# Kernel optimization log

Measured on AMD Instinct MI355X. Metric: run time of the kernel, lower is better.

The kernel has to match this reference:

```python
import jax, jax.numpy as jnp
import numpy as np

P = 8.0  # Lp exponent of the distance neuron (finite-p stage of l_inf-dist training)


def _patches(t, k, stride, pad):
    # [B, Cin, H, W] -> [B, Cin*k*k, H', W'], feature dim ordered channel-major
    return jax.lax.conv_general_dilated_patches(
        t, (k, k), (stride, stride), [(pad, pad), (pad, pad)])


def _lp(d):
    # d: [B, Cout, Cin*k*k, H', W'] nonnegative -> Lp norm over patch dim
    return jnp.power(jnp.sum(jnp.power(d, P), axis=2), 1.0 / P)


def norm_dist_conv(x, l, u, w, stride, pad):
    # Lp-distance "convolution": y[b,o,i,j] = || patch(x)[b,:,i,j] - w[o,:] ||_p
    # mean_normalize=True: zero-center each output unit's weight vector
    Cout, Cin, k, _ = w.shape
    wf = w.reshape(Cout, -1)
    wf = wf - jnp.mean(wf, axis=1, keepdims=True)
    wb = wf[None, :, :, None, None]                      # [1, Cout, Ckk, 1, 1]
    px = _patches(x, k, stride, pad)[:, None]            # [B, 1, Ckk, H', W']
    pl = _patches(l, k, stride, pad)[:, None]
    pu = _patches(u, k, stride, pad)[:, None]
    y = _lp(jnp.abs(px - wb))
    # interval bounds of |x_j - w_j| given x_j in [l_j, u_j], then monotone Lp
    dl = jnp.maximum(jnp.maximum(pl - wb, wb - pu), 0.0)
    du = jnp.maximum(jnp.abs(pl - wb), jnp.abs(pu - wb))
    return y, _lp(dl), _lp(du)


def bound_relu(x, l, u):
    # ReLU is monotone: apply elementwise to value and both bounds
    return jax.nn.relu(x), jax.nn.relu(l), jax.nn.relu(u)


def setup_inputs() -> dict:
    key = jax.random.key(0)
    k1, k2, k3 = jax.random.split(key, 3)
    B, C, H, W = 4, 32, 32, 32
    eps = 0.1  # l_inf perturbation radius
    x = jax.random.normal(k1, (B, C, H, W), dtype=jnp.float32)
    lower = x - eps
    upper = x + eps
    scale = 1.0 / np.sqrt(C * 9)
    weight1 = jax.random.normal(k2, (C, C, 3, 3), dtype=jnp.float32) * scale
    weight2 = jax.random.normal(k3, (C, C, 3, 3), dtype=jnp.float32) * scale
    return {"x": x, "lower": lower, "upper": upper,
            "weight1": weight1, "weight2": weight2}


def reference(x, lower, upper, weight1, weight2):
    # conv1 (stride=1, pad=1) -> BoundReLU -> conv2 -> residual add -> BoundReLU
    o = norm_dist_conv(x, lower, upper, weight1, 1, 1)
    o = bound_relu(*o)
    o = norm_dist_conv(*o, weight2, 1, 1)
    out = (o[0] + x, o[1] + lower, o[2] + upper)  # identity shortcut (stride=1, in==out)
    out = bound_relu(*out)
    return jnp.stack(out)  # [3, B, C, H, W]: (value, lower, upper)
```

## Files before the change

### kernel.cpp

```cpp
#include <hip/hip_runtime.h>

#define NB 4
#define NC 32
#define NH 32
#define NW 32
#define KK 288
#define PLANE (NB*NC*NH*NW)
#define CQ 8

typedef float v2f __attribute__((ext_vector_type(2)));

__device__ __forceinline__ float s3(float v) { return sqrtf(sqrtf(sqrtf(v))); }
__device__ __forceinline__ v2f pkfma(v2f a, v2f b, v2f c) { return __builtin_elementwise_fma(a, b, c); }
__device__ __forceinline__ v2f pkmax(v2f a, v2f b) { return __builtin_elementwise_max(a, b); }

__global__ __launch_bounds__(256) void prep_weights_k(
        const float* __restrict__ w1, const float* __restrict__ w2,
        float* __restrict__ wf1, float* __restrict__ wf2)
{
    const int row = blockIdx.x;
    const float* src = (row < NC) ? w1 : w2;
    float* dst = (row < NC) ? wf1 : wf2;
    const int co = row & (NC - 1);
    const int tid = threadIdx.x;
    __shared__ float red[256];
    const float a = src[co*KK + tid];
    const float b = (tid + 256 < KK) ? src[co*KK + tid + 256] : 0.0f;
    red[tid] = a + b;
    __syncthreads();
    for (int s = 128; s > 0; s >>= 1) {
        if (tid < s) red[tid] += red[tid + s];
        __syncthreads();
    }
    const float mean = red[0] * (1.0f / (float)KK);
    const int q    = ((co >> 4) << 3) | (co & 7);
    const int slot = (co >> 3) & 1;
    {
        const int e = tid, c = e / 9, r9 = e - c*9, r = r9 / 3, kw = r9 - r*3;
        dst[((q*NC + c)*3 + r)*8 + kw*2 + slot] = a - mean;
    }
    if (tid + 256 < KK) {
        const int e = tid + 256, c = e / 9, r9 = e - c*9, r = r9 / 3, kw = r9 - r*3;
        dst[((q*NC + c)*3 + r)*8 + kw*2 + slot] = b - mean;
    }
}

template<bool STAGE2>
__global__ __launch_bounds__(256, 2) void normdist_conv_k(
    const float* __restrict__ sy,
    const float* __restrict__ sl,
    const float* __restrict__ su,
    const float* __restrict__ wf,
    float* __restrict__ pY, float* __restrict__ pL, float* __restrict__ pU)
{
    const int h    = blockIdx.x;
    const int cq   = blockIdx.y;
    const int cq0  = cq * CQ;
    const int b    = blockIdx.z;
    const int tid  = threadIdx.x;
    const int wv   = tid >> 6;
    const int lane = tid & 63;
    const int ps   = lane >> 4;
    const int pp   = lane & 15;
    const int p0   = pp * 2;

    __shared__ float4 sP[CQ*3*34];

    for (int i = tid; i < CQ*3*34; i += 256) {
        const int c   = i / 102;
        const int rem = i - c*102;
        const int r   = rem / 34;
        const int col = rem - r*34;
        const int gh  = h + r - 1;
        const int gw  = col - 1;
        float vx = 0.0f, vl = 0.0f, vu = 0.0f;
        if ((unsigned)gh < NH && (unsigned)gw < NW) {
            const int g = ((b*NC + cq0 + c)*NH + gh)*NW + gw;
            if (STAGE2) {
                vx = s3(sy[g] + sy[PLANE + g] + sy[2*PLANE + g] + sy[3*PLANE + g]);
                vl = s3(sl[g] + sl[PLANE + g] + sl[2*PLANE + g] + sl[3*PLANE + g]);
                vu = s3(su[g] + su[PLANE + g] + su[2*PLANE + g] + su[3*PLANE + g]);
            } else {
                vx = sy[g]; vl = sl[g]; vu = su[g];
            }
        }
        sP[i] = make_float4(vx, vl, vu, 0.0f);
    }
    __syncthreads();

    const int q = wv*4 + ps;
    const float4* wq = (const float4*)wf + (q*NC + cq0)*6;

    v2f aY0 = {0,0}, aL0 = {0,0}, aU0 = {0,0};
    v2f aY1 = {0,0}, aL1 = {0,0}, aU1 = {0,0};

    auto tap2 = [&](v2f w, const float4& p, v2f& aY, v2f& aL, v2f& aU) {
        const v2f P  = {p.x, p.x};
        const v2f Lo = {p.y, p.y};
        const v2f Up = {p.z, p.z};
        const v2f d  = P - w;
        const v2f d2 = d*d, d4 = d2*d2;
        aY = pkfma(d4, d4, aY);
        const v2f a  = Lo - w;
        const v2f nb = w - Up;
        const v2f z  = {0.0f, 0.0f};
        const v2f m  = pkmax(pkmax(a, nb), z);
        const v2f m2 = m*m, m4 = m2*m2;
        aL = pkfma(m4, m4, aL);
        const v2f a2 = a*a, q2 = nb*nb;
        const v2f mm2 = pkmax(a2, q2);
        const v2f mm4 = mm2*mm2;
        aU = pkfma(mm4, mm4, aU);
    };

    for (int c = 0; c < CQ; ++c) {
        const int pb = c*102 + p0;
        const float4 p00 = sP[pb +  0], p01 = sP[pb +  1], p02 = sP[pb +  2], p03 = sP[pb +  3];
        const float4 p10 = sP[pb + 34], p11 = sP[pb + 35], p12 = sP[pb + 36], p13 = sP[pb + 37];
        const float4 p20 = sP[pb + 68], p21 = sP[pb + 69], p22 = sP[pb + 70], p23 = sP[pb + 71];

        const float4 w0lo = wq[c*6+0], w0hi = wq[c*6+1];
        const float4 w1lo = wq[c*6+2], w1hi = wq[c*6+3];
        const float4 w2lo = wq[c*6+4], w2hi = wq[c*6+5];

        const v2f w00 = {w0lo.x, w0lo.y}, w01 = {w0lo.z, w0lo.w}, w02 = {w0hi.x, w0hi.y};
        const v2f w10 = {w1lo.x, w1lo.y}, w11 = {w1lo.z, w1lo.w}, w12 = {w1hi.x, w1hi.y};
        const v2f w20 = {w2lo.x, w2lo.y}, w21 = {w2lo.z, w2lo.w}, w22 = {w2hi.x, w2hi.y};

        tap2(w00, p00, aY0, aL0, aU0); tap2(w01, p01, aY0, aL0, aU0); tap2(w02, p02, aY0, aL0, aU0);
        tap2(w10, p10, aY0, aL0, aU0); tap2(w11, p11, aY0, aL0, aU0); tap2(w12, p12, aY0, aL0, aU0);
        tap2(w20, p20, aY0, aL0, aU0); tap2(w21, p21, aY0, aL0, aU0); tap2(w22, p22, aY0, aL0, aU0);
        tap2(w00, p01, aY1, aL1, aU1); tap2(w01, p02, aY1, aL1, aU1); tap2(w02, p03, aY1, aL1, aU1);
        tap2(w10, p11, aY1, aL1, aU1); tap2(w11, p12, aY1, aL1, aU1); tap2(w12, p13, aY1, aL1, aU1);
        tap2(w20, p21, aY1, aL1, aU1); tap2(w21, p22, aY1, aL1, aU1); tap2(w22, p23, aY1, aL1, aU1);
    }

    const int co0 = ((q >> 3) << 4) | (q & 7);
    const int o   = ((b*NC + co0)*NH + h)*NW + p0;
    const int o1  = o + 8*NH*NW;

    float* dY = pY + cq*PLANE;
    float* dL = pL + cq*PLANE;
    float* dU = pU + cq*PLANE;
    *(float2*)&dY[o]  = make_float2(aY0.x, aY1.x);
    *(float2*)&dY[o1] = make_float2(aY0.y, aY1.y);
    *(float2*)&dL[o]  = make_float2(aL0.x, aL1.x);
    *(float2*)&dL[o1] = make_float2(aL0.y, aL1.y);
    *(float2*)&dU[o]  = make_float2(aU0.x, aU1.x);
    *(float2*)&dU[o1] = make_float2(aU0.y, aU1.y);
}

__global__ __launch_bounds__(256) void epilogue_k(
    const float* __restrict__ pY, const float* __restrict__ pL, const float* __restrict__ pU,
    const float* __restrict__ x,  const float* __restrict__ l,  const float* __restrict__ u,
    float* __restrict__ out)
{
    const int i = blockIdx.x*256 + threadIdx.x;
    const float4* pY4 = (const float4*)pY;
    const float4* pL4 = (const float4*)pL;
    const float4* pU4 = (const float4*)pU;
    const float4* x4  = (const float4*)x;
    const float4* l4  = (const float4*)l;
    const float4* u4  = (const float4*)u;
    float4* out4 = (float4*)out;
    const int Q = PLANE/4;

    const float4 ya = pY4[i], yb = pY4[Q+i], yc = pY4[2*Q+i], yd = pY4[3*Q+i];
    const float4 la = pL4[i], lb = pL4[Q+i], lc = pL4[2*Q+i], ld = pL4[3*Q+i];
    const float4 ua = pU4[i], ub = pU4[Q+i], uc = pU4[2*Q+i], ud = pU4[3*Q+i];
    const float4 xr = x4[i], lr = l4[i], ur = u4[i];

    float4 oy, ol, ou;
    oy.x = fmaxf(s3(ya.x+yb.x+yc.x+yd.x) + xr.x, 0.0f);
    oy.y = fmaxf(s3(ya.y+yb.y+yc.y+yd.y) + xr.y, 0.0f);
    oy.z = fmaxf(s3(ya.z+yb.z+yc.z+yd.z) + xr.z, 0.0f);
    oy.w = fmaxf(s3(ya.w+yb.w+yc.w+yd.w) + xr.w, 0.0f);
    ol.x = fmaxf(s3(la.x+lb.x+lc.x+ld.x) + lr.x, 0.0f);
    ol.y = fmaxf(s3(la.y+lb.y+lc.y+ld.y) + lr.y, 0.0f);
    ol.z = fmaxf(s3(la.z+lb.z+lc.z+ld.z) + lr.z, 0.0f);
    ol.w = fmaxf(s3(la.w+lb.w+lc.w+ld.w) + lr.w, 0.0f);
    ou.x = fmaxf(s3(ua.x+ub.x+uc.x+ud.x) + ur.x, 0.0f);
    ou.y = fmaxf(s3(ua.y+ub.y+uc.y+ud.y) + ur.y, 0.0f);
    ou.z = fmaxf(s3(ua.z+ub.z+uc.z+ud.z) + ur.z, 0.0f);
    ou.w = fmaxf(s3(ua.w+ub.w+uc.w+ud.w) + ur.w, 0.0f);

    out4[i]       = oy;
    out4[Q + i]   = ol;
    out4[2*Q + i] = ou;
}

extern "C" void kernel_launch(void* const* d_in, const int* in_sizes, int n_in,
                              void* d_out, int out_size, void* d_ws, size_t ws_size,
                              hipStream_t stream)
{
    const float* x  = (const float*)d_in[0];
    const float* l  = (const float*)d_in[1];
    const float* u  = (const float*)d_in[2];
    const float* w1 = (const float*)d_in[3];
    const float* w2 = (const float*)d_in[4];
    float* ws  = (float*)d_ws;
    float* wf1 = ws;
    float* wf2 = wf1 + 12288;
    float* p1Y = wf2 + 12288;
    float* p1L = p1Y + 4*PLANE;
    float* p1U = p1L + 4*PLANE;
    float* p2Y = p1U + 4*PLANE;
    float* p2L = p2Y + 4*PLANE;
    float* p2U = p2L + 4*PLANE;
    float* out = (float*)d_out;

    prep_weights_k<<<64, 256, 0, stream>>>(w1, w2, wf1, wf2);

    dim3 grd(NH, 4, NB);
    normdist_conv_k<false><<<grd, 256, 0, stream>>>(x, l, u, wf1, p1Y, p1L, p1U);
    normdist_conv_k<true ><<<grd, 256, 0, stream>>>(p1Y, p1L, p1U, wf2, p2Y, p2L, p2U);
    epilogue_k<<<PLANE/1024, 256, 0, stream>>>(p2Y, p2L, p2U, x, l, u, out);
}
```

Before: 103.3 us.

## Assign one output pixel per thread with 512-thread conv blocks

The conv kernel now uses 512 threads per block, and each thread computes one output column for a channel pair instead of two adjacent columns. This doubles thread-level parallelism and cuts per-thread registers and accumulators, which should raise occupancy. The cost is losing the reuse of the overlapping patch loads between the two neighbouring pixels, so shared-memory and weight loads per FLOP go up. Stores also shrink from float2 to scalar.

After: 100.2 us, median of 2. 3.0% less time.

```diff
diff --git a/kernel.cpp b/kernel.cpp
--- a/kernel.cpp
+++ b/kernel.cpp
@@ -46,7 +46,7 @@
 }
 
 template<bool STAGE2>
-__global__ __launch_bounds__(256, 2) void normdist_conv_k(
+__global__ __launch_bounds__(512, 4) void normdist_conv_k(
     const float* __restrict__ sy,
     const float* __restrict__ sl,
     const float* __restrict__ su,
@@ -60,13 +60,12 @@
     const int tid  = threadIdx.x;
     const int wv   = tid >> 6;
     const int lane = tid & 63;
-    const int ps   = lane >> 4;
-    const int pp   = lane & 15;
-    const int p0   = pp * 2;
+    const int q    = wv*2 + (lane >> 5);
+    const int px   = lane & 31;
 
     __shared__ float4 sP[CQ*3*34];
 
-    for (int i = tid; i < CQ*3*34; i += 256) {
+    for (int i = tid; i < CQ*3*34; i += 512) {
         const int c   = i / 102;
         const int rem = i - c*102;
         const int r   = rem / 34;
@@ -88,13 +87,11 @@
     }
     __syncthreads();
 
-    const int q = wv*4 + ps;
     const float4* wq = (const float4*)wf + (q*NC + cq0)*6;
 
-    v2f aY0 = {0,0}, aL0 = {0,0}, aU0 = {0,0};
-    v2f aY1 = {0,0}, aL1 = {0,0}, aU1 = {0,0};
-
-    auto tap2 = [&](v2f w, const float4& p, v2f& aY, v2f& aL, v2f& aU) {
+    v2f aY = {0,0}, aL = {0,0}, aU = {0,0};
+
+    auto tap2 = [&](v2f w, const float4& p) {
         const v2f P  = {p.x, p.x};
         const v2f Lo = {p.y, p.y};
         const v2f Up = {p.z, p.z};
@@ -114,40 +111,30 @@
     };
 
     for (int c = 0; c < CQ; ++c) {
-        const int pb = c*102 + p0;
-        const float4 p00 = sP[pb +  0], p01 = sP[pb +  1], p02 = sP[pb +  2], p03 = sP[pb +  3];
-        const float4 p10 = sP[pb + 34], p11 = sP[pb + 35], p12 = sP[pb + 36], p13 = sP[pb + 37];
-        const float4 p20 = sP[pb + 68], p21 = sP[pb + 69], p22 = sP[pb + 70], p23 = sP[pb + 71];
+        const int pb = c*102 + px;
+        const float4 p00 = sP[pb +  0], p01 = sP[pb +  1], p02 = sP[pb +  2];
+        const float4 p10 = sP[pb + 34], p11 = sP[pb + 35], p12 = sP[pb + 36];
+        const float4 p20 = sP[pb + 68], p21 = sP[pb + 69], p22 = sP[pb + 70];
 
         const float4 w0lo = wq[c*6+0], w0hi = wq[c*6+1];
         const float4 w1lo = wq[c*6+2], w1hi = wq[c*6+3];
         const float4 w2lo = wq[c*6+4], w2hi = wq[c*6+5];
 
-        const v2f w00 = {w0lo.x, w0lo.y}, w01 = {w0lo.z, w0lo.w}, w02 = {w0hi.x, w0hi.y};
-        const v2f w10 = {w1lo.x, w1lo.y}, w11 = {w1lo.z, w1lo.w}, w12 = {w1hi.x, w1hi.y};
-        const v2f w20 = {w2lo.x, w2lo.y}, w21 = {w2lo.z, w2lo.w}, w22 = {w2hi.x, w2hi.y};
-
-        tap2(w00, p00, aY0, aL0, aU0); tap2(w01, p01, aY0, aL0, aU0); tap2(w02, p02, aY0, aL0, aU0);
-        tap2(w10, p10, aY0, aL0, aU0); tap2(w11, p11, aY0, aL0, aU0); tap2(w12, p12, aY0, aL0, aU0);
-        tap2(w20, p20, aY0, aL0, aU0); tap2(w21, p21, aY0, aL0, aU0); tap2(w22, p22, aY0, aL0, aU0);
-        tap2(w00, p01, aY1, aL1, aU1); tap2(w01, p02, aY1, aL1, aU1); tap2(w02, p03, aY1, aL1, aU1);
-        tap2(w10, p11, aY1, aL1, aU1); tap2(w11, p12, aY1, aL1, aU1); tap2(w12, p13, aY1, aL1, aU1);
-        tap2(w20, p21, aY1, aL1, aU1); tap2(w21, p22, aY1, aL1, aU1); tap2(w22, p23, aY1, aL1, aU1);
+        tap2((v2f){w0lo.x, w0lo.y}, p00); tap2((v2f){w0lo.z, w0lo.w}, p01); tap2((v2f){w0hi.x, w0hi.y}, p02);
+        tap2((v2f){w1lo.x, w1lo.y}, p10); tap2((v2f){w1lo.z, w1lo.w}, p11); tap2((v2f){w1hi.x, w1hi.y}, p12);
+        tap2((v2f){w2lo.x, w2lo.y}, p20); tap2((v2f){w2lo.z, w2lo.w}, p21); tap2((v2f){w2hi.x, w2hi.y}, p22);
     }
 
     const int co0 = ((q >> 3) << 4) | (q & 7);
-    const int o   = ((b*NC + co0)*NH + h)*NW + p0;
+    const int o   = ((b*NC + co0)*NH + h)*NW + px;
     const int o1  = o + 8*NH*NW;
 
     float* dY = pY + cq*PLANE;
     float* dL = pL + cq*PLANE;
     float* dU = pU + cq*PLANE;
-    *(float2*)&dY[o]  = make_float2(aY0.x, aY1.x);
-    *(float2*)&dY[o1] = make_float2(aY0.y, aY1.y);
-    *(float2*)&dL[o]  = make_float2(aL0.x, aL1.x);
-    *(float2*)&dL[o1] = make_float2(aL0.y, aL1.y);
-    *(float2*)&dU[o]  = make_float2(aU0.x, aU1.x);
-    *(float2*)&dU[o1] = make_float2(aU0.y, aU1.y);
+    dY[o]  = aY.x;  dY[o1] = aY.y;
+    dL[o]  = aL.x;  dL[o1] = aL.y;
+    dU[o]  = aU.x;  dU[o1] = aU.y;
 }
 
 __global__ __launch_bounds__(256) void epilogue_k(
@@ -212,7 +199,7 @@
     prep_weights_k<<<64, 256, 0, stream>>>(w1, w2, wf1, wf2);
 
     dim3 grd(NH, 4, NB);
-    normdist_conv_k<false><<<grd, 256, 0, stream>>>(x, l, u, wf1, p1Y, p1L, p1U);
-    normdist_conv_k<true ><<<grd, 256, 0, stream>>>(p1Y, p1L, p1U, wf2, p2Y, p2L, p2U);
+    normdist_conv_k<false><<<grd, 512, 0, stream>>>(x, l, u, wf1, p1Y, p1L, p1U);
+    normdist_conv_k<true ><<<grd, 512, 0, stream>>>(p1Y, p1L, p1U, wf2, p2Y, p2L, p2U);
     epilogue_k<<<PLANE/1024, 256, 0, stream>>>(p2Y, p2L, p2U, x, l, u, out);
 }
```
